# Performance work log

Hardware: AMD Instinct MI355X
Metric: run time of the kernel (lower is better)

The kernel has to match this reference:

```python
import jax, jax.numpy as jnp
import numpy as np
import math

EPS_LN = 1e-5
TARGET_ACTIVITY = 0.1
THETA = 2.0 ** 16

B, NH, T, D, N = 2, 12, 2048, 768, 256


def layernorm(x):
    m = jnp.mean(x, axis=-1, keepdims=True)
    v = jnp.mean((x - m) ** 2, axis=-1, keepdims=True)
    return (x - m) / jnp.sqrt(v + EPS_LN)


def get_freqs(n):
    q = jnp.floor(jnp.arange(n, dtype=jnp.float32) / 2.0) * 2.0  # quantize by 2
    return 1.0 / (THETA ** (q / n)) / (2.0 * math.pi)


def rope(phases, v):
    ph = (phases % 1.0) * (2.0 * math.pi)
    c, s = jnp.cos(ph), jnp.sin(ph)
    even = v[..., 0::2]
    odd = v[..., 1::2]
    v_rot = jnp.stack((-odd, even), axis=-1).reshape(v.shape)  # interleaved rotate
    return v * c + v_rot * s


def setup_inputs() -> dict:
    key = jax.random.key(0)
    ks = jax.random.split(key, 5)
    std = 0.02
    return {
        "x": jax.random.normal(ks[0], (B, 1, T, D), dtype=jnp.float32),
        "encoder": jax.random.normal(ks[1], (NH, D, N), dtype=jnp.float32) * std,
        "encoder_v": jax.random.normal(ks[2], (NH, D, N), dtype=jnp.float32) * std,
        "decoder": jax.random.normal(ks[3], (NH * N, D), dtype=jnp.float32) * std,
        "scale": jnp.ones((D,), dtype=jnp.float32),
        "running_activity": jnp.ones((D,), dtype=jnp.float32) * TARGET_ACTIVITY,
    }


def reference(x, encoder, encoder_v, decoder, scale, running_activity):
    Bv, _, Tv, Dv = x.shape
    nh, _, Nv = encoder.shape

    # encode + ReLU sparsify: [B,1,T,D] @ [nh,D,N] -> [B,nh,T,N]
    x_latent = jnp.einsum('bztd,hdn->bhtn', x, encoder)
    x_sparse = jax.nn.relu(x_latent)

    # RoPE on Q=K=x_sparse
    freqs = get_freqs(Nv)  # [N]
    r_phases = jnp.arange(Tv, dtype=jnp.float32)[:, None] * freqs[None, :]  # [T,N]
    QR = rope(r_phases, x_sparse)
    KR = rope(r_phases, x_sparse)

    # non-softmax causal attention, strictly lower-triangular (diag=-1)
    scores = jnp.einsum('bhtn,bhsn->bhts', QR, KR)
    mask = jnp.tril(jnp.ones((Tv, Tv), dtype=scores.dtype), k=-1)
    scores = scores * mask
    yKV = jnp.einsum('bhts,bsd->bhtd', scores, x[:, 0])  # V = x

    yKV = layernorm(yKV)
    y_sparse = jax.nn.relu(jnp.einsum('bhtd,hdn->bhtn', yKV, encoder_v))
    xy_sparse = x_sparse * y_sparse  # [B,nh,T,N]; dropout=0 (eval)

    # [B,nh,T,N] -> [B,1,T,nh*N] @ [nh*N,D]
    flat = jnp.transpose(xy_sparse, (0, 2, 1, 3)).reshape(Bv, 1, Tv, nh * Nv)
    yMLP = flat @ decoder

    y = layernorm(yMLP)
    regulation = TARGET_ACTIVITY / (running_activity + 1e-6)
    y = y * jnp.sqrt(regulation) * scale

    return layernorm(x + y), xy_sparse
```

## Files before the change

### kernel.cpp

```cpp
#include <hip/hip_runtime.h>
#include <math.h>

#define TT 2048
#define DD 768
#define NN 256
#define NHH 12
#define BB 2
#define CH 512

typedef unsigned short u16;
typedef __attribute__((ext_vector_type(8))) short bf16x8;
typedef __attribute__((ext_vector_type(8))) unsigned short u16x8;
typedef __attribute__((ext_vector_type(4))) float f32x4;

static inline int imin(int a, int b) { return a < b ? a : b; }

__device__ __forceinline__ u16 f2b(float f) {
  union { float f; unsigned u; } a; a.f = f;
  unsigned r = a.u + 0x7FFF + ((a.u >> 16) & 1);
  return (u16)(r >> 16);
}
__device__ __forceinline__ float b2f(u16 h) {
  union { unsigned u; float f; } a; a.u = ((unsigned)h) << 16;
  return a.f;
}

__device__ __forceinline__ void async16(const void* g, void* l) {
  __builtin_amdgcn_global_load_lds(
      (const __attribute__((address_space(1))) unsigned*)g,
      (__attribute__((address_space(3))) unsigned*)l, 16, 0, 0);
}

#define KSWZ(row) (((row) >> 1) & 3)

__device__ __forceinline__ void stage128x32(
    const u16* __restrict__ gbase, size_t ld, u16* lds, int tid) {
  const int w = tid >> 6, l = tid & 63;
#pragma unroll
  for (int q = 0; q < 2; ++q) {
    const int row = w * 32 + q * 16 + (l >> 2);
    const int kc = ((l & 3) ^ KSWZ(row)) << 3;
    async16(gbase + (size_t)row * ld + kc, lds + (w * 32 + q * 16) * 32);
  }
}

__device__ __forceinline__ void stage64x32(
    const u16* __restrict__ gbase, size_t ld, u16* lds, int tid) {
  const int w = tid >> 6, l = tid & 63;
  const int row = w * 16 + (l >> 2);
  const int kc = ((l & 3) ^ KSWZ(row)) << 3;
  async16(gbase + (size_t)row * ld + kc, lds + w * 512);
}

__device__ __forceinline__ void mfma_step(
    const u16* As, const u16* Bs, int wr, int wc, int lane, f32x4 acc[4][4]) {
  const int m16 = lane & 15, quad = lane >> 4;
  bf16x8 a[4], b[4];
#pragma unroll
  for (int i = 0; i < 4; ++i) {
    const int row = wr * 64 + i * 16 + m16;
    a[i] = *(const bf16x8*)&As[row * 32 + ((quad ^ KSWZ(row)) << 3)];
  }
#pragma unroll
  for (int j = 0; j < 4; ++j) {
    const int row = wc * 64 + j * 16 + m16;
    b[j] = *(const bf16x8*)&Bs[row * 32 + ((quad ^ KSWZ(row)) << 3)];
  }
#pragma unroll
  for (int i = 0; i < 4; ++i)
#pragma unroll
    for (int j = 0; j < 4; ++j)
      acc[i][j] = __builtin_amdgcn_mfma_f32_16x16x32_bf16(a[i], b[j], acc[i][j], 0, 0, 0);
}

__device__ __forceinline__ void copy_out128(
    const u16* buf, u16* g, size_t ld, int tid) {
#pragma unroll
  for (int s = 0; s < 8; ++s) {
    const int off = (s * 256 + tid) * 8;
    const int row = off >> 7, col = off & 127;
    *(u16x8*)&g[(size_t)row * ld + col] = *(const u16x8*)&buf[off];
  }
}

#define GEMM_PROLOGUE()                                            \
  __shared__ __attribute__((aligned(16))) u16 smem[32768];         \
  const int tid = threadIdx.x;                                     \
  const int w = tid >> 6, lane = tid & 63;                         \
  const int wr = w >> 1, wc = w & 1;                               \
  const int col16 = lane & 15, quad = lane >> 4;                   \
  f32x4 acc[4][4];                                                 \
  _Pragma("unroll") for (int i = 0; i < 4; ++i)                    \
  _Pragma("unroll") for (int j = 0; j < 4; ++j)                    \
      acc[i][j] = (f32x4){0.f, 0.f, 0.f, 0.f};

#define PIPELINED_K_LOOP64(ABASE, ALD, BBASE, BLD, KTOT)                    \
  {                                                                         \
    stage128x32((ABASE), (ALD), smem, tid);                                 \
    stage128x32((ABASE) + 32, (ALD), smem + 4096, tid);                     \
    stage128x32((BBASE), (BLD), smem + 8192, tid);                          \
    stage128x32((BBASE) + 32, (BLD), smem + 12288, tid);                    \
    const int np_ = (KTOT) / 64;                                            \
    for (int pp_ = 0; pp_ < np_; ++pp_) {                                   \
      u16* cb_ = (pp_ & 1) ? smem + 16384 : smem;                           \
      u16* nb_ = (pp_ & 1) ? smem : smem + 16384;                           \
      if (pp_ + 1 < np_) {                                                  \
        const int kn_ = (pp_ + 1) * 64;                                     \
        stage128x32((ABASE) + kn_, (ALD), nb_, tid);                        \
        stage128x32((ABASE) + kn_ + 32, (ALD), nb_ + 4096, tid);            \
        stage128x32((BBASE) + kn_, (BLD), nb_ + 8192, tid);                 \
        stage128x32((BBASE) + kn_ + 32, (BLD), nb_ + 12288, tid);           \
        asm volatile("s_waitcnt vmcnt(8)" ::: "memory");                    \
      } else {                                                              \
        asm volatile("s_waitcnt vmcnt(0)" ::: "memory");                    \
      }                                                                     \
      __builtin_amdgcn_s_barrier();                                         \
      __builtin_amdgcn_sched_barrier(0);                                    \
      mfma_step(cb_, cb_ + 8192, wr, wc, lane, acc);                        \
      mfma_step(cb_ + 4096, cb_ + 12288, wr, wc, lane, acc);                \
      __builtin_amdgcn_sched_barrier(0);                                    \
      __builtin_amdgcn_s_barrier();                                         \
    }                                                                       \
  }

__device__ __forceinline__ void tcvt_body(
    const float* __restrict__ ip, u16* __restrict__ op, int R, int C,
    int bx, int by, int tid, float (*tile)[33]) {
  const int c0 = bx * 32, r0 = by * 32;
  const int tx = tid & 31, ty = tid >> 5;
#pragma unroll
  for (int p = 0; p < 4; ++p)
    tile[ty + p * 8][tx] = ip[(size_t)(r0 + ty + p * 8) * C + c0 + tx];
  __syncthreads();
#pragma unroll
  for (int p = 0; p < 4; ++p)
    op[(size_t)(c0 + ty + p * 8) * R + r0 + tx] = f2b(tile[tx][ty + p * 8]);
}

__global__ __launch_bounds__(256) void k_prep(
    const float* __restrict__ x, u16* __restrict__ X16, u16* __restrict__ XT16,
    const float* __restrict__ enc, u16* __restrict__ ENCT,
    const float* __restrict__ encv, u16* __restrict__ ENCVT,
    const float* __restrict__ dec, u16* __restrict__ DECT,
    float2* __restrict__ CS) {
  __shared__ float tile[32][33];
  const int tid = threadIdx.x;
  const int bid = blockIdx.x;
  if (bid < 3072) {
    const size_t i = ((size_t)bid * 256 + tid) * 4;
    float4 v = *(const float4*)&x[i];
    u16 o[4] = {f2b(v.x), f2b(v.y), f2b(v.z), f2b(v.w)};
    *(ushort4*)&X16[i] = *(ushort4*)o;
  } else if (bid < 6144) {
    const int b = bid - 3072;
    const int bz = b / 1536, rb = b % 1536;
    tcvt_body(x + (size_t)bz * TT * DD, XT16 + (size_t)bz * DD * TT,
              TT, DD, rb % 24, rb / 24, tid, tile);
  } else if (bid < 8448) {
    const int b = bid - 6144;
    const int bz = b / 192, rb = b % 192;
    tcvt_body(enc + (size_t)bz * DD * NN, ENCT + (size_t)bz * NN * DD,
              DD, NN, rb % 8, rb / 8, tid, tile);
  } else if (bid < 10752) {
    const int b = bid - 8448;
    const int bz = b / 192, rb = b % 192;
    tcvt_body(encv + (size_t)bz * DD * NN, ENCVT + (size_t)bz * NN * DD,
              DD, NN, rb % 8, rb / 8, tid, tile);
  } else if (bid < 13056) {
    const int b = bid - 10752;
    tcvt_body(dec, DECT, NHH * NN, DD, b % 24, b / 24, tid, tile);
  } else {
    const int idx = (bid - 13056) * 256 + tid;
    const int t = idx >> 7, n2 = idx & 127;
    const float freq = exp2f((float)(2 * n2) * -0.0625f) * 0.15915494309189535f;
    const float phase = (float)t * freq;
    const float ph = (phase - floorf(phase)) * 6.283185307179586f;
    CS[idx] = make_float2(__cosf(ph), __sinf(ph));
  }
}

__global__ __launch_bounds__(256) void k_colsum(
    const u16* __restrict__ encvt, float* __restrict__ colsum) {
  const int row = blockIdx.x * 4 + (threadIdx.x >> 6);
  const int lane = threadIdx.x & 63;
  const u16* pr = encvt + (size_t)row * DD;
  float s = 0.f;
#pragma unroll
  for (int i = 0; i < 3; ++i) {
    ushort4 v = *(const ushort4*)&pr[(lane << 2) + i * 256];
    s += b2f(v.x) + b2f(v.y) + b2f(v.z) + b2f(v.w);
  }
#pragma unroll
  for (int off = 32; off; off >>= 1) s += __shfl_xor(s, off);
  if (lane == 0) colsum[row] = s;
}

__device__ __forceinline__ int swz8(int row) { return ((row >> 3) & 7) << 3; }

__global__ __launch_bounds__(256) void k1_encode(
    const u16* __restrict__ x16, const u16* __restrict__ enct,
    const float2* __restrict__ CS,
    u16* __restrict__ qr16, u16* __restrict__ qrt16) {
  const int h = blockIdx.z;
  const int m0 = blockIdx.x * 128, n0 = blockIdx.y * 128;
  GEMM_PROLOGUE();
  PIPELINED_K_LOOP64(x16 + (size_t)m0 * DD, DD,
                     enct + ((size_t)h * NN + n0) * DD, DD, DD);
  __syncthreads();
#pragma unroll
  for (int i = 0; i < 4; ++i)
#pragma unroll
    for (int j = 0; j < 4; ++j) {
      const int n = n0 + wc * 64 + j * 16 + col16;
      float rv[4], pv[4];
#pragma unroll
      for (int r = 0; r < 4; ++r) rv[r] = fmaxf(acc[i][j][r], 0.f);
#pragma unroll
      for (int r = 0; r < 4; ++r) pv[r] = __shfl_xor(rv[r], 1);
#pragma unroll
      for (int r = 0; r < 4; ++r) {
        const int lrow = wr * 64 + i * 16 + quad * 4 + r;
        const int t = (m0 + lrow) & (TT - 1);
        const float2 cs = CS[t * 128 + (n >> 1)];
        const float o = (n & 1) ? (rv[r] * cs.x + pv[r] * cs.y)
                                : (rv[r] * cs.x - pv[r] * cs.y);
        smem[lrow * 128 + ((wc * 64 + j * 16 + col16) ^ swz8(lrow))] = f2b(o);
      }
    }
  __syncthreads();
  const int bq = m0 >> 11, tb = m0 & (TT - 1);
  const size_t sl = (size_t)(bq * NHH + h);
  u16* qg = qr16 + (sl * TT + tb) * NN + n0;
#pragma unroll
  for (int s = 0; s < 8; ++s) {
    const int off = (s * 256 + tid) * 8;
    const int row = off >> 7, col = off & 127;
    *(u16x8*)&qg[(size_t)row * NN + col] =
        *(const u16x8*)&smem[row * 128 + (col ^ swz8(row))];
  }
#pragma unroll
  for (int s = 0; s < 8; ++s) {
    const int off = (s * 256 + tid) * 8;
    const int nr = off >> 7, tc = off & 127;
    const int sw = swz8(tc);
    u16 vals[8];
#pragma unroll
    for (int k = 0; k < 8; ++k) vals[k] = smem[(tc + k) * 128 + (nr ^ sw)];
    *(u16x8*)&qrt16[(sl * NN + n0 + nr) * TT + tb + tc] = *(u16x8*)vals;
  }
}

__global__ __launch_bounds__(256) void kS_band(
    const u16* __restrict__ qr16, u16* __restrict__ sb, int bh0) {
  const int z = blockIdx.y;
  const int bh = bh0 + z;
  const int cc = blockIdx.x / 10, rr = blockIdx.x % 10;
  int i = (int)((sqrtf(8.f * rr + 1.f) - 1.f) * 0.5f);
  while ((i + 1) * (i + 2) / 2 <= rr) ++i;
  while (i * (i + 1) / 2 > rr) --i;
  const int j = rr - i * (i + 1) / 2;
  const int t0 = (cc * 4 + i) * 128;
  const int s0 = cc * CH + j * 128;
  const u16* q = qr16 + (size_t)bh * TT * NN;
  GEMM_PROLOGUE();
  PIPELINED_K_LOOP64(q + (size_t)t0 * NN, NN, q + (size_t)s0 * NN, NN, NN);
  const bool diag = (i == j);
  __syncthreads();
#pragma unroll
  for (int ii = 0; ii < 4; ++ii)
#pragma unroll
    for (int jj = 0; jj < 4; ++jj) {
      const int s = s0 + wc * 64 + jj * 16 + col16;
#pragma unroll
      for (int r = 0; r < 4; ++r) {
        const int lrow = wr * 64 + ii * 16 + quad * 4 + r;
        const int t = t0 + lrow;
        float v = acc[ii][jj][r];
        if (diag && s >= t) v = 0.f;
        smem[lrow * 128 + wc * 64 + jj * 16 + col16] = f2b(v);
      }
    }
  __syncthreads();
  copy_out128(smem, sb + ((size_t)z * TT + t0) * CH + j * 128, CH, tid);
}

__global__ __launch_bounds__(256) void kB_all(
    const u16* __restrict__ xt16, const u16* __restrict__ qrt16,
    u16* __restrict__ h16, int bh0) {
  __shared__ __attribute__((aligned(16))) u16 sm[32768];
  u16* buf0 = sm;
  u16* buf1 = sm + 12288;
  u16* snap = sm + 24576;
  const int tid = threadIdx.x;
  const int w = tid >> 6, lane = tid & 63;
  const int m16 = lane & 15, quad = lane >> 4;
  const int z = blockIdx.z;
  const int bh = bh0 + z, b = bh / NHH;
  const int d0 = blockIdx.x * 64, n0 = blockIdx.y * 128;
  f32x4 acc[4][2];
#pragma unroll
  for (int i = 0; i < 4; ++i)
#pragma unroll
    for (int j = 0; j < 2; ++j) acc[i][j] = (f32x4){0.f, 0.f, 0.f, 0.f};
  const u16* Ab = xt16 + ((size_t)b * DD + d0) * TT;
  const u16* Bb = qrt16 + ((size_t)bh * NN + n0) * TT;
#define KB_STAGE(buf, k0)                                                   \
  {                                                                         \
    stage64x32(Ab + (k0), TT, (buf), tid);                                  \
    stage64x32(Ab + (k0) + 32, TT, (buf) + 2048, tid);                      \
    stage128x32(Bb + (k0), TT, (buf) + 4096, tid);                          \
    stage128x32(Bb + (k0) + 32, TT, (buf) + 8192, tid);                     \
  }
  for (int c = 0; c < 3; ++c) {
    const int kbase = c * CH;
    KB_STAGE(buf0, kbase);
    for (int s = 0; s < CH / 64; ++s) {
      u16* cb = (s & 1) ? buf1 : buf0;
      u16* nb = (s & 1) ? buf0 : buf1;
      if (s + 1 < CH / 64) {
        KB_STAGE(nb, kbase + (s + 1) * 64);
        asm volatile("s_waitcnt vmcnt(6)" ::: "memory");
      } else {
        asm volatile("s_waitcnt vmcnt(0)" ::: "memory");
      }
      __builtin_amdgcn_s_barrier();
      __builtin_amdgcn_sched_barrier(0);
#pragma unroll
      for (int half = 0; half < 2; ++half) {
        bf16x8 a[4], bb[2];
#pragma unroll
        for (int i = 0; i < 4; ++i) {
          const int row = i * 16 + m16;
          a[i] = *(const bf16x8*)&cb[half * 2048 + row * 32 +
                                     ((quad ^ KSWZ(row)) << 3)];
        }
#pragma unroll
        for (int j = 0; j < 2; ++j) {
          const int row = w * 32 + j * 16 + m16;
          bb[j] = *(const bf16x8*)&cb[4096 + half * 4096 + row * 32 +
                                      ((quad ^ KSWZ(row)) << 3)];
        }
#pragma unroll
        for (int i = 0; i < 4; ++i)
#pragma unroll
          for (int j = 0; j < 2; ++j)
            acc[i][j] = __builtin_amdgcn_mfma_f32_16x16x32_bf16(a[i], bb[j], acc[i][j], 0, 0, 0);
      }
      __builtin_amdgcn_sched_barrier(0);
      __builtin_amdgcn_s_barrier();
    }
#pragma unroll
    for (int i = 0; i < 4; ++i)
#pragma unroll
      for (int j = 0; j < 2; ++j)
#pragma unroll
        for (int r = 0; r < 4; ++r)
          snap[(i * 16 + quad * 4 + r) * 128 + w * 32 + j * 16 + m16] =
              f2b(acc[i][j][r]);
    __syncthreads();
    u16* hd = h16 + (size_t)(z * 3 + c) * DD * NN;
#pragma unroll
    for (int s4 = 0; s4 < 4; ++s4) {
      const int off = (s4 * 256 + tid) * 8;
      const int row = off >> 7, col = off & 127;
      *(u16x8*)&hd[(size_t)(d0 + row) * NN + n0 + col] = *(const u16x8*)&snap[off];
    }
    __syncthreads();
  }
#undef KB_STAGE
}

__device__ static const int TTORD[16] = {15, 11, 7, 14, 10, 6, 13, 9,
                                         5, 3, 12, 8, 4, 2, 1, 0};

__global__ __launch_bounds__(256) void kA_attn(
    const u16* __restrict__ qr16, const u16* __restrict__ h16,
    const u16* __restrict__ sb, const u16* __restrict__ xt16,
    u16* __restrict__ ykv16, float2* __restrict__ PART, int gsTT, int bh0) {
  __shared__ __attribute__((aligned(16))) u16 smem[32768];
  const int tid = threadIdx.x;
  const int w = tid >> 6, lane = tid & 63;
  const int wr = w >> 1, wc = w & 1;
  const int col16 = lane & 15, quad = lane >> 4;
  const int nwg = gridDim.x;
  const int bid = blockIdx.x;
  const int qn = nwg >> 3, r8 = nwg & 7;
  const int xcd = bid & 7, pos = bid >> 3;
  const int wg = (xcd < r8 ? xcd * (qn + 1) : r8 * (qn + 1) + (xcd - r8) * qn) + pos;
  const int z = wg / 96;
  const int tt = TTORD[(wg / 6) & 15];
  const int dblk = wg % 6;
  const int d0 = dblk * 128;
  const int bh = bh0 + z, b = bh / NHH;
  const int c = tt >> 2, it = tt & 3;
  const int t0 = tt * 128;
  f32x4 acc[4][4];
#pragma unroll
  for (int i = 0; i < 4; ++i)
#pragma unroll
    for (int j = 0; j < 4; ++j) acc[i][j] = (f32x4){0.f, 0.f, 0.f, 0.f};

  const int c4 = (c > 0) ? 4 : 0;
  const int nP = c4 + (it + 1) * 2;
  const u16* hs = h16 + ((size_t)(z * 3 + (c > 0 ? c - 1 : 0)) * DD + d0) * NN;
  const u16* qb = qr16 + ((size_t)bh * TT + t0) * NN;
  const u16* sbb = sb + ((size_t)z * TT + t0) * CH;
  const u16* xb = xt16 + ((size_t)b * DD + d0) * TT + c * CH;

#define KA_STAGE(buf, p)                                                  \
  {                                                                       \
    const u16 *pa_, *pb_; size_t la_, lb_;                                \
    if ((p) < c4) {                                                       \
      pa_ = qb + (p) * 64; la_ = NN;                                      \
      pb_ = hs + (p) * 64; lb_ = NN;                                      \
    } else {                                                              \
      const int q_ = (p) - c4;                                            \
      const int j_ = q_ >> 1, kk_ = (q_ & 1) << 6;                        \
      pa_ = sbb + j_ * 128 + kk_; la_ = CH;                               \
      pb_ = xb + j_ * 128 + kk_; lb_ = TT;                                \
    }                                                                     \
    stage128x32(pa_, la_, (buf), tid);                                    \
    stage128x32(pa_ + 32, la_, (buf) + 4096, tid);                        \
    stage128x32(pb_, lb_, (buf) + 8192, tid);                             \
    stage128x32(pb_ + 32, lb_, (buf) + 12288, tid);                       \
  }

  u16* bufA = smem;
  u16* bufB = smem + 16384;
  KA_STAGE(bufA, 0);
  for (int p = 0; p < nP; ++p) {
    u16* cb = (p & 1) ? bufB : bufA;
    u16* nb = (p & 1) ? bufA : bufB;
    if (p + 1 < nP) {
      KA_STAGE(nb, p + 1);
      asm volatile("s_waitcnt vmcnt(8)" ::: "memory");
    } else {
      asm volatile("s_waitcnt vmcnt(0)" ::: "memory");
    }
    __builtin_amdgcn_s_barrier();
    __builtin_amdgcn_sched_barrier(0);
    mfma_step(cb, cb + 8192, wr, wc, lane, acc);
    mfma_step(cb + 4096, cb + 12288, wr, wc, lane, acc);
    __builtin_amdgcn_sched_barrier(0);
    __builtin_amdgcn_s_barrier();
  }
#undef KA_STAGE

  __syncthreads();
#pragma unroll
  for (int i = 0; i < 4; ++i)
#pragma unroll
    for (int j = 0; j < 4; ++j)
#pragma unroll
      for (int r = 0; r < 4; ++r) {
        const int lrow = wr * 64 + i * 16 + quad * 4 + r;
        smem[lrow * 128 + wc * 64 + j * 16 + col16] = f2b(acc[i][j][r]);
      }
  __syncthreads();
  float2* scratch = (float2*)&smem[16384];
  u16* yg = ykv16 + ((size_t)z * TT + t0) * DD + d0;
#pragma unroll
  for (int s = 0; s < 8; ++s) {
    const int off = (s * 256 + tid) * 8;
    const int row = off >> 7, col = off & 127;
    const u16x8 v = *(const u16x8*)&smem[off];
    *(u16x8*)&yg[(size_t)row * DD + col] = v;
    float ps = 0.f, pq = 0.f;
#pragma unroll
    for (int k = 0; k < 8; ++k) {
      const float f = b2f(v[k]);
      ps += f;
      pq += f * f;
    }
    scratch[row * 17 + (tid & 15)] = make_float2(ps, pq);
  }
  __syncthreads();
  if (tid < 128) {
    const float2* pr = &scratch[tid * 17];
    float s = 0.f, q2 = 0.f;
#pragma unroll
    for (int k = 0; k < 16; ++k) { s += pr[k].x; q2 += pr[k].y; }
    PART[(size_t)dblk * gsTT + z * TT + t0 + tid] = make_float2(s, q2);
  }
}

__global__ __launch_bounds__(256) void k3r_stats(
    const float2* __restrict__ PART, float* __restrict__ mu,
    float* __restrict__ rs, int gsTT) {
  const int row = blockIdx.x * 256 + threadIdx.x;
  float s = 0.f, q = 0.f;
#pragma unroll
  for (int d = 0; d < 6; ++d) {
    const float2 p2 = PART[(size_t)d * gsTT + row];
    s += p2.x;
    q += p2.y;
  }
  const float m = s * (1.f / 768.f);
  mu[row] = m;
  rs[row] = rsqrtf(q * (1.f / 768.f) - m * m + 1e-5f);
}

__global__ __launch_bounds__(256) void k4_xy(
    const u16* __restrict__ ykv16, const u16* __restrict__ encvt,
    const float2* __restrict__ CS,
    u16* __restrict__ qrxy, const float* __restrict__ mu,
    const float* __restrict__ rs, const float* __restrict__ colsum,
    float* __restrict__ out2, int bh0) {
  const int z = blockIdx.z;
  const int bh = bh0 + z, h = bh % NHH;
  const int t0 = blockIdx.x * 128, n0 = blockIdx.y * 128;
  GEMM_PROLOGUE();
  PIPELINED_K_LOOP64(ykv16 + ((size_t)z * TT + t0) * DD, DD,
                     encvt + ((size_t)h * NN + n0) * DD, DD, DD);
  {
    const u16* qg = qrxy + ((size_t)bh * TT + t0) * NN + n0;
#pragma unroll
    for (int s = 0; s < 8; ++s) {
      const int row = s * 16 + w * 4 + (lane >> 4);
      const int col = (lane & 15) * 8;
      async16(qg + (size_t)row * NN + col,
              smem + 16384 + (s * 256 + w * 64) * 8);
    }
  }
  asm volatile("s_waitcnt vmcnt(0)" ::: "memory");
  __syncthreads();
#pragma unroll
  for (int i = 0; i < 4; ++i) {
    float muv[4], rsv[4];
#pragma unroll
    for (int r = 0; r < 4; ++r) {
      const int grow = z * TT + t0 + wr * 64 + i * 16 + quad * 4 + r;
      muv[r] = mu[grow];
      rsv[r] = rs[grow];
    }
#pragma unroll
    for (int j = 0; j < 4; ++j) {
      const int lcol = wc * 64 + j * 16 + col16;
      const int n = n0 + lcol;
      const float csum = colsum[h * NN + n];
#pragma unroll
      for (int r = 0; r < 4; ++r) {
        const int lrow = wr * 64 + i * 16 + quad * 4 + r;
        const int t = t0 + lrow;
        const float ys = fmaxf(rsv[r] * acc[i][j][r] - rsv[r] * muv[r] * csum, 0.f);
        const unsigned pq =
            *(const unsigned*)&smem[16384 + lrow * 128 + (lcol & ~1)];
        const float lo = b2f((u16)pq), hi = b2f((u16)(pq >> 16));
        const float2 cs = CS[t * 128 + (n >> 1)];
        const float xs = (n & 1) ? (hi * cs.x - lo * cs.y)
                                 : (lo * cs.x + hi * cs.y);
        const float val = ys * xs;
        out2[((size_t)bh * TT + t) * NN + n] = val;
        smem[lrow * 128 + lcol] = f2b(val);
      }
    }
  }
  __syncthreads();
  copy_out128(smem, qrxy + ((size_t)bh * TT + t0) * NN + n0, NN, tid);
}

__global__ __launch_bounds__(256) void k5_mlp(
    const u16* __restrict__ xyq, const u16* __restrict__ dect,
    float* __restrict__ ymlp) {
  __shared__ __attribute__((aligned(16))) u16 sm[24576];
  const int tid = threadIdx.x;
  const int w = tid >> 6, lane = tid & 63;
  const int wr = w >> 1, wc = w & 1;
  const int m16 = lane & 15, quad = lane >> 4;
  const int m0 = blockIdx.x * 64, d0 = blockIdx.y * 64;
  f32x4 acc[2][2];
#pragma unroll
  for (int i = 0; i < 2; ++i)
#pragma unroll
    for (int j = 0; j < 2; ++j) acc[i][j] = (f32x4){0.f, 0.f, 0.f, 0.f};
  const int ar = w * 16 + (lane >> 2);
  const int m = m0 + ar;
  const int b = m >> 11, t = m & (TT - 1);
  const int kc = (((lane & 3) ^ KSWZ(ar)) << 3);
#define K5_STAGE(buf, k0)                                                   \
  {                                                                         \
    const int hh_ = (k0) >> 8;                                              \
    const int kk_ = ((k0) & 255) + kc;                                      \
    const u16* ap_ = xyq + ((size_t)(b * NHH + hh_) * TT + t) * NN;         \
    async16(ap_ + kk_, (buf) + w * 512);                                    \
    async16(ap_ + kk_ + 32, (buf) + 2048 + w * 512);                        \
    stage64x32(dect + (size_t)d0 * (NHH * NN) + (k0), NHH * NN,             \
               (buf) + 4096, tid);                                          \
    stage64x32(dect + (size_t)d0 * (NHH * NN) + (k0) + 32, NHH * NN,        \
               (buf) + 6144, tid);                                          \
  }
  const int NK = (NHH * NN) / 64;
  u16 *b0 = sm, *b1 = sm + 8192, *b2 = sm + 16384;
  K5_STAGE(b0, 0);
  K5_STAGE(b1, 64);
  for (int s = 0; s < NK; ++s) {
    if (s + 2 < NK) {
      K5_STAGE(b2, (s + 2) * 64);
      asm volatile("s_waitcnt vmcnt(8)" ::: "memory");
    } else if (s + 1 < NK) {
      asm volatile("s_waitcnt vmcnt(4)" ::: "memory");
    } else {
      asm volatile("s_waitcnt vmcnt(0)" ::: "memory");
    }
    __builtin_amdgcn_s_barrier();
    __builtin_amdgcn_sched_barrier(0);
#pragma unroll
    for (int half = 0; half < 2; ++half) {
      bf16x8 a[2], bb[2];
#pragma unroll
      for (int i = 0; i < 2; ++i) {
        const int row = wr * 32 + i * 16 + m16;
        a[i] = *(const bf16x8*)&b0[half * 2048 + row * 32 +
                                   ((quad ^ KSWZ(row)) << 3)];
      }
#pragma unroll
      for (int j = 0; j < 2; ++j) {
        const int row = wc * 32 + j * 16 + m16;
        bb[j] = *(const bf16x8*)&b0[4096 + half * 2048 + row * 32 +
                                    ((quad ^ KSWZ(row)) << 3)];
      }
#pragma unroll
      for (int i = 0; i < 2; ++i)
#pragma unroll
        for (int j = 0; j < 2; ++j)
          acc[i][j] = __builtin_amdgcn_mfma_f32_16x16x32_bf16(a[i], bb[j], acc[i][j], 0, 0, 0);
    }
    __builtin_amdgcn_sched_barrier(0);
    __builtin_amdgcn_s_barrier();
    u16* tmp = b0; b0 = b1; b1 = b2; b2 = tmp;
  }
#undef K5_STAGE
#pragma unroll
  for (int i = 0; i < 2; ++i)
#pragma unroll
    for (int j = 0; j < 2; ++j) {
      const int d = d0 + wc * 32 + j * 16 + m16;
#pragma unroll
      for (int r = 0; r < 4; ++r) {
        const int mm = m0 + wr * 32 + i * 16 + quad * 4 + r;
        ymlp[(size_t)mm * DD + d] = acc[i][j][r];
      }
    }
}

__global__ __launch_bounds__(256) void k6_final(
    const float* __restrict__ ymlp, const float* __restrict__ x,
    const float* __restrict__ scale, const float* __restrict__ ra,
    float* __restrict__ out1) {
  const int row = blockIdx.x;
  const int tid = threadIdx.x;
  const int wid = tid >> 6, lane = tid & 63;
  __shared__ float red[8];
  float v[3];
  float sum = 0.f, sq = 0.f;
#pragma unroll
  for (int j = 0; j < 3; ++j) {
    v[j] = ymlp[(size_t)row * DD + tid + j * 256];
    sum += v[j]; sq += v[j] * v[j];
  }
#pragma unroll
  for (int off = 32; off; off >>= 1) { sum += __shfl_xor(sum, off); sq += __shfl_xor(sq, off); }
  if (lane == 0) { red[wid] = sum; red[4 + wid] = sq; }
  __syncthreads();
  sum = red[0] + red[1] + red[2] + red[3];
  sq = red[4] + red[5] + red[6] + red[7];
  const float m1 = sum * (1.f / 768.f);
  const float r1 = rsqrtf(sq * (1.f / 768.f) - m1 * m1 + 1e-5f);
  float z[3];
  float sum2 = 0.f, sq2 = 0.f;
#pragma unroll
  for (int j = 0; j < 3; ++j) {
    const int d = tid + j * 256;
    float y = (v[j] - m1) * r1 * sqrtf(0.1f / (ra[d] + 1e-6f)) * scale[d];
    z[j] = x[(size_t)row * DD + d] + y;
    sum2 += z[j]; sq2 += z[j] * z[j];
  }
  __syncthreads();
#pragma unroll
  for (int off = 32; off; off >>= 1) { sum2 += __shfl_xor(sum2, off); sq2 += __shfl_xor(sq2, off); }
  if (lane == 0) { red[wid] = sum2; red[4 + wid] = sq2; }
  __syncthreads();
  sum2 = red[0] + red[1] + red[2] + red[3];
  sq2 = red[4] + red[5] + red[6] + red[7];
  const float m2 = sum2 * (1.f / 768.f);
  const float r2 = rsqrtf(sq2 * (1.f / 768.f) - m2 * m2 + 1e-5f);
#pragma unroll
  for (int j = 0; j < 3; ++j)
    out1[(size_t)row * DD + tid + j * 256] = (z[j] - m2) * r2;
}

extern "C" void kernel_launch(void* const* d_in, const int* in_sizes, int n_in,
                              void* d_out, int out_size, void* d_ws, size_t ws_size,
                              hipStream_t stream) {
  const float* x = (const float*)d_in[0];
  const float* enc = (const float*)d_in[1];
  const float* encv = (const float*)d_in[2];
  const float* dec = (const float*)d_in[3];
  const float* scale = (const float*)d_in[4];
  const float* ra = (const float*)d_in[5];
  float* out1 = (float*)d_out;
  float* out2 = out1 + (size_t)BB * TT * DD;
  float* ymlp = out1;

  const int NS = BB * NHH;
  unsigned char* p = (unsigned char*)d_ws;
  u16* X16 = (u16*)p;    p += (size_t)BB * TT * DD * 2;
  u16* XT16 = (u16*)p;   p += (size_t)BB * DD * TT * 2;
  u16* ENCT = (u16*)p;   p += (size_t)NHH * NN * DD * 2;
  u16* ENCVT = (u16*)p;  p += (size_t)NHH * NN * DD * 2;
  u16* DECT = (u16*)p;   p += (size_t)DD * NHH * NN * 2;
  u16* QR16 = (u16*)p;   p += (size_t)NS * TT * NN * 2;
  u16* QRT16 = (u16*)p;  p += (size_t)NS * NN * TT * 2;
  float* COLSUM = (float*)p; p += (size_t)NHH * NN * 4;
  float2* CS = (float2*)p;   p += (size_t)TT * (NN / 2) * sizeof(float2);
  const size_t SLICE_B = (size_t)TT * CH * 2 + 3 * (size_t)DD * NN * 2 +
                         (size_t)TT * DD * 2 + (size_t)TT * 56;
  size_t fixed = (size_t)(p - (unsigned char*)d_ws);
  size_t rem = (ws_size > fixed) ? ws_size - fixed : 0;
  int GSmax = (int)(rem / SLICE_B);
  if (GSmax < 1) GSmax = 1;
  if (GSmax > NS) GSmax = NS;
  const int ngrp = (NS + GSmax - 1) / GSmax;
  const int GS = (NS + ngrp - 1) / ngrp;
  u16* SB = (u16*)p;     p += (size_t)GS * TT * CH * 2;
  u16* H16 = (u16*)p;    p += (size_t)GS * 3 * DD * NN * 2;
  u16* YKV16 = (u16*)p;  p += (size_t)GS * TT * DD * 2;
  float2* PART = (float2*)p; p += (size_t)GS * TT * 6 * sizeof(float2);
  float* MU = (float*)p; p += (size_t)GS * TT * 4;
  float* RS = (float*)p; p += (size_t)GS * TT * 4;
  const int gsTT = GS * TT;

  k_prep<<<dim3(14080), 256, 0, stream>>>(
      x, X16, XT16, enc, ENCT, encv, ENCVT, dec, DECT, CS);
  k_colsum<<<dim3(NHH * NN / 4), 256, 0, stream>>>(ENCVT, COLSUM);

  k1_encode<<<dim3(BB * TT / 128, NN / 128, NHH), 256, 0, stream>>>(
      X16, ENCT, CS, QR16, QRT16);

  for (int bh0 = 0; bh0 < NS; bh0 += GS) {
    const int gs = imin(GS, NS - bh0);
    kS_band<<<dim3(40, gs), 256, 0, stream>>>(QR16, SB, bh0);
    kB_all<<<dim3(DD / 64, NN / 128, gs), 256, 0, stream>>>(
        XT16, QRT16, H16, bh0);
    kA_attn<<<dim3(96 * gs), 256, 0, stream>>>(
        QR16, H16, SB, XT16, YKV16, PART, gsTT, bh0);
    k3r_stats<<<dim3(gs * TT / 256), 256, 0, stream>>>(PART, MU, RS, gsTT);
    k4_xy<<<dim3(TT / 128, NN / 128, gs), 256, 0, stream>>>(
        YKV16, ENCVT, CS, QR16, MU, RS, COLSUM, out2, bh0);
  }

  k5_mlp<<<dim3(BB * TT / 64, DD / 64), 256, 0, stream>>>(QR16, DECT, ymlp);
  k6_final<<<dim3(BB * TT), 256, 0, stream>>>(ymlp, x, scale, ra, out1);
}
```

Measured before the change: 356.2 us.

## Merge band and H kernels, fold stats into k4, retile MLP GEMM

Combines the banded score kernel and the H-projection kernel into a single launch that dispatches on block index, so their blocks share the GPU and one launch is saved. It removes the separate row-statistics kernel by having k4_xy reduce the six partial sums itself, which drops the MU/RS buffers. It also retiles the decoder MLP GEMM from 64x64 to 128x128 tiles with double buffering and a swizzled block order. The trade-offs are redundant partial-sum reads in k4, fewer MLP blocks (192), and a mixed-workload kernel whose blocks run different code paths.

```diff
diff --git a/kernel.cpp b/kernel.cpp
--- a/kernel.cpp
+++ b/kernel.cpp
@@ -83,8 +83,10 @@
   }
 }
 
-#define GEMM_PROLOGUE()                                            \
-  __shared__ __attribute__((aligned(16))) u16 smem[32768];         \
+#define GEMM_SMEM \
+  __shared__ __attribute__((aligned(16))) u16 smem[32768];
+
+#define GEMM_VARS()                                                \
   const int tid = threadIdx.x;                                     \
   const int w = tid >> 6, lane = tid & 63;                         \
   const int wr = w >> 1, wc = w & 1;                               \
@@ -93,6 +95,8 @@
   _Pragma("unroll") for (int i = 0; i < 4; ++i)                    \
   _Pragma("unroll") for (int j = 0; j < 4; ++j)                    \
       acc[i][j] = (f32x4){0.f, 0.f, 0.f, 0.f};
+
+#define GEMM_PROLOGUE() GEMM_SMEM GEMM_VARS()
 
 #define PIPELINED_K_LOOP64(ABASE, ALD, BBASE, BLD, KTOT)                    \
   {                                                                         \
@@ -250,60 +254,65 @@
   }
 }
 
-__global__ __launch_bounds__(256) void kS_band(
-    const u16* __restrict__ qr16, u16* __restrict__ sb, int bh0) {
-  const int z = blockIdx.y;
-  const int bh = bh0 + z;
-  const int cc = blockIdx.x / 10, rr = blockIdx.x % 10;
-  int i = (int)((sqrtf(8.f * rr + 1.f) - 1.f) * 0.5f);
-  while ((i + 1) * (i + 2) / 2 <= rr) ++i;
-  while (i * (i + 1) / 2 > rr) --i;
-  const int j = rr - i * (i + 1) / 2;
-  const int t0 = (cc * 4 + i) * 128;
-  const int s0 = cc * CH + j * 128;
-  const u16* q = qr16 + (size_t)bh * TT * NN;
-  GEMM_PROLOGUE();
-  PIPELINED_K_LOOP64(q + (size_t)t0 * NN, NN, q + (size_t)s0 * NN, NN, NN);
-  const bool diag = (i == j);
-  __syncthreads();
-#pragma unroll
-  for (int ii = 0; ii < 4; ++ii)
-#pragma unroll
-    for (int jj = 0; jj < 4; ++jj) {
-      const int s = s0 + wc * 64 + jj * 16 + col16;
-#pragma unroll
-      for (int r = 0; r < 4; ++r) {
-        const int lrow = wr * 64 + ii * 16 + quad * 4 + r;
-        const int t = t0 + lrow;
-        float v = acc[ii][jj][r];
-        if (diag && s >= t) v = 0.f;
-        smem[lrow * 128 + wc * 64 + jj * 16 + col16] = f2b(v);
-      }
-    }
-  __syncthreads();
-  copy_out128(smem, sb + ((size_t)z * TT + t0) * CH + j * 128, CH, tid);
-}
-
-__global__ __launch_bounds__(256) void kB_all(
-    const u16* __restrict__ xt16, const u16* __restrict__ qrt16,
-    u16* __restrict__ h16, int bh0) {
-  __shared__ __attribute__((aligned(16))) u16 sm[32768];
-  u16* buf0 = sm;
-  u16* buf1 = sm + 12288;
-  u16* snap = sm + 24576;
+__global__ __launch_bounds__(256) void kSB(
+    const u16* __restrict__ qr16, const u16* __restrict__ xt16,
+    const u16* __restrict__ qrt16, u16* __restrict__ sb,
+    u16* __restrict__ h16, int nS, int bh0) {
+  GEMM_SMEM;
   const int tid = threadIdx.x;
   const int w = tid >> 6, lane = tid & 63;
-  const int m16 = lane & 15, quad = lane >> 4;
-  const int z = blockIdx.z;
-  const int bh = bh0 + z, b = bh / NHH;
-  const int d0 = blockIdx.x * 64, n0 = blockIdx.y * 128;
-  f32x4 acc[4][2];
-#pragma unroll
-  for (int i = 0; i < 4; ++i)
-#pragma unroll
-    for (int j = 0; j < 2; ++j) acc[i][j] = (f32x4){0.f, 0.f, 0.f, 0.f};
-  const u16* Ab = xt16 + ((size_t)b * DD + d0) * TT;
-  const u16* Bb = qrt16 + ((size_t)bh * NN + n0) * TT;
+  const int col16 = lane & 15, quad = lane >> 4;
+  if ((int)blockIdx.x < nS) {
+    const int wr = w >> 1, wc = w & 1;
+    const int z = blockIdx.x / 40, sub = blockIdx.x % 40;
+    const int bh = bh0 + z;
+    const int cc = sub / 10, rr = sub % 10;
+    int i = (int)((sqrtf(8.f * rr + 1.f) - 1.f) * 0.5f);
+    while ((i + 1) * (i + 2) / 2 <= rr) ++i;
+    while (i * (i + 1) / 2 > rr) --i;
+    const int j = rr - i * (i + 1) / 2;
+    const int t0 = (cc * 4 + i) * 128;
+    const int s0 = cc * CH + j * 128;
+    const u16* q = qr16 + (size_t)bh * TT * NN;
+    f32x4 acc[4][4];
+#pragma unroll
+    for (int a = 0; a < 4; ++a)
+#pragma unroll
+      for (int b = 0; b < 4; ++b) acc[a][b] = (f32x4){0.f, 0.f, 0.f, 0.f};
+    PIPELINED_K_LOOP64(q + (size_t)t0 * NN, NN, q + (size_t)s0 * NN, NN, NN);
+    const bool diag = (i == j);
+    __syncthreads();
+#pragma unroll
+    for (int ii = 0; ii < 4; ++ii)
+#pragma unroll
+      for (int jj = 0; jj < 4; ++jj) {
+        const int s = s0 + wc * 64 + jj * 16 + col16;
+#pragma unroll
+        for (int r = 0; r < 4; ++r) {
+          const int lrow = wr * 64 + ii * 16 + quad * 4 + r;
+          const int t = t0 + lrow;
+          float v = acc[ii][jj][r];
+          if (diag && s >= t) v = 0.f;
+          smem[lrow * 128 + wc * 64 + jj * 16 + col16] = f2b(v);
+        }
+      }
+    __syncthreads();
+    copy_out128(smem, sb + ((size_t)z * TT + t0) * CH + j * 128, CH, tid);
+  } else {
+    const int r2 = blockIdx.x - nS;
+    const int z = r2 / 24, rr2 = r2 % 24;
+    const int d0 = (rr2 % 12) * 64, n0 = (rr2 / 12) * 128;
+    const int bh = bh0 + z, b = bh / NHH;
+    u16* buf0 = smem;
+    u16* buf1 = smem + 12288;
+    u16* snap = smem + 24576;
+    f32x4 acc[4][2];
+#pragma unroll
+    for (int i = 0; i < 4; ++i)
+#pragma unroll
+      for (int j = 0; j < 2; ++j) acc[i][j] = (f32x4){0.f, 0.f, 0.f, 0.f};
+    const u16* Ab = xt16 + ((size_t)b * DD + d0) * TT;
+    const u16* Bb = qrt16 + ((size_t)bh * NN + n0) * TT;
 #define KB_STAGE(buf, k0)                                                   \
   {                                                                         \
     stage64x32(Ab + (k0), TT, (buf), tid);                                  \
@@ -311,63 +320,64 @@
     stage128x32(Bb + (k0), TT, (buf) + 4096, tid);                          \
     stage128x32(Bb + (k0) + 32, TT, (buf) + 8192, tid);                     \
   }
-  for (int c = 0; c < 3; ++c) {
-    const int kbase = c * CH;
-    KB_STAGE(buf0, kbase);
-    for (int s = 0; s < CH / 64; ++s) {
-      u16* cb = (s & 1) ? buf1 : buf0;
-      u16* nb = (s & 1) ? buf0 : buf1;
-      if (s + 1 < CH / 64) {
-        KB_STAGE(nb, kbase + (s + 1) * 64);
-        asm volatile("s_waitcnt vmcnt(6)" ::: "memory");
-      } else {
-        asm volatile("s_waitcnt vmcnt(0)" ::: "memory");
+    for (int c = 0; c < 3; ++c) {
+      const int kbase = c * CH;
+      KB_STAGE(buf0, kbase);
+      for (int s = 0; s < CH / 64; ++s) {
+        u16* cb = (s & 1) ? buf1 : buf0;
+        u16* nb = (s & 1) ? buf0 : buf1;
+        if (s + 1 < CH / 64) {
+          KB_STAGE(nb, kbase + (s + 1) * 64);
+          asm volatile("s_waitcnt vmcnt(6)" ::: "memory");
+        } else {
+          asm volatile("s_waitcnt vmcnt(0)" ::: "memory");
+        }
+        __builtin_amdgcn_s_barrier();
+        __builtin_amdgcn_sched_barrier(0);
+#pragma unroll
+        for (int half = 0; half < 2; ++half) {
+          bf16x8 a[4], bb[2];
+#pragma unroll
+          for (int i = 0; i < 4; ++i) {
+            const int row = i * 16 + col16;
+            a[i] = *(const bf16x8*)&cb[half * 2048 + row * 32 +
+                                       ((quad ^ KSWZ(row)) << 3)];
+          }
+#pragma unroll
+          for (int j = 0; j < 2; ++j) {
+            const int row = w * 32 + j * 16 + col16;
+            bb[j] = *(const bf16x8*)&cb[4096 + half * 4096 + row * 32 +
+                                        ((quad ^ KSWZ(row)) << 3)];
+          }
+#pragma unroll
+          for (int i = 0; i < 4; ++i)
+#pragma unroll
+            for (int j = 0; j < 2; ++j)
+              acc[i][j] = __builtin_amdgcn_mfma_f32_16x16x32_bf16(a[i], bb[j], acc[i][j], 0, 0, 0);
+        }
+        __builtin_amdgcn_sched_barrier(0);
+        __builtin_amdgcn_s_barrier();
       }
-      __builtin_amdgcn_s_barrier();
-      __builtin_amdgcn_sched_barrier(0);
-#pragma unroll
-      for (int half = 0; half < 2; ++half) {
-        bf16x8 a[4], bb[2];
-#pragma unroll
-        for (int i = 0; i < 4; ++i) {
-          const int row = i * 16 + m16;
-          a[i] = *(const bf16x8*)&cb[half * 2048 + row * 32 +
-                                     ((quad ^ KSWZ(row)) << 3)];
-        }
-#pragma unroll
-        for (int j = 0; j < 2; ++j) {
-          const int row = w * 32 + j * 16 + m16;
-          bb[j] = *(const bf16x8*)&cb[4096 + half * 4096 + row * 32 +
-                                      ((quad ^ KSWZ(row)) << 3)];
-        }
-#pragma unroll
-        for (int i = 0; i < 4; ++i)
-#pragma unroll
-          for (int j = 0; j < 2; ++j)
-            acc[i][j] = __builtin_amdgcn_mfma_f32_16x16x32_bf16(a[i], bb[j], acc[i][j], 0, 0, 0);
+#pragma unroll
+      for (int i = 0; i < 4; ++i)
+#pragma unroll
+        for (int j = 0; j < 2; ++j)
+#pragma unroll
+          for (int r = 0; r < 4; ++r)
+            snap[(i * 16 + quad * 4 + r) * 128 + w * 32 + j * 16 + col16] =
+                f2b(acc[i][j][r]);
+      __syncthreads();
+      u16* hd = h16 + (size_t)(z * 3 + c) * DD * NN;
+#pragma unroll
+      for (int s4 = 0; s4 < 4; ++s4) {
+        const int off = (s4 * 256 + tid) * 8;
+        const int row = off >> 7, col = off & 127;
+        *(u16x8*)&hd[(size_t)(d0 + row) * NN + n0 + col] = *(const u16x8*)&snap[off];
       }
-      __builtin_amdgcn_sched_barrier(0);
-      __builtin_amdgcn_s_barrier();
-    }
-#pragma unroll
-    for (int i = 0; i < 4; ++i)
-#pragma unroll
-      for (int j = 0; j < 2; ++j)
-#pragma unroll
-        for (int r = 0; r < 4; ++r)
-          snap[(i * 16 + quad * 4 + r) * 128 + w * 32 + j * 16 + m16] =
-              f2b(acc[i][j][r]);
-    __syncthreads();
-    u16* hd = h16 + (size_t)(z * 3 + c) * DD * NN;
-#pragma unroll
-    for (int s4 = 0; s4 < 4; ++s4) {
-      const int off = (s4 * 256 + tid) * 8;
-      const int row = off >> 7, col = off & 127;
-      *(u16x8*)&hd[(size_t)(d0 + row) * NN + n0 + col] = *(const u16x8*)&snap[off];
-    }
-    __syncthreads();
-  }
+      __syncthreads();
+    }
 #undef KB_STAGE
+  }
 }
 
 __device__ static const int TTORD[16] = {15, 11, 7, 14, 10, 6, 13, 9,
@@ -377,7 +387,7 @@
     const u16* __restrict__ qr16, const u16* __restrict__ h16,
     const u16* __restrict__ sb, const u16* __restrict__ xt16,
     u16* __restrict__ ykv16, float2* __restrict__ PART, int gsTT, int bh0) {
-  __shared__ __attribute__((aligned(16))) u16 smem[32768];
+  GEMM_SMEM;
   const int tid = threadIdx.x;
   const int w = tid >> 6, lane = tid & 63;
   const int wr = w >> 1, wc = w & 1;
@@ -484,28 +494,12 @@
   }
 }
 
-__global__ __launch_bounds__(256) void k3r_stats(
-    const float2* __restrict__ PART, float* __restrict__ mu,
-    float* __restrict__ rs, int gsTT) {
-  const int row = blockIdx.x * 256 + threadIdx.x;
-  float s = 0.f, q = 0.f;
-#pragma unroll
-  for (int d = 0; d < 6; ++d) {
-    const float2 p2 = PART[(size_t)d * gsTT + row];
-    s += p2.x;
-    q += p2.y;
-  }
-  const float m = s * (1.f / 768.f);
-  mu[row] = m;
-  rs[row] = rsqrtf(q * (1.f / 768.f) - m * m + 1e-5f);
-}
-
 __global__ __launch_bounds__(256) void k4_xy(
     const u16* __restrict__ ykv16, const u16* __restrict__ encvt,
     const float2* __restrict__ CS,
-    u16* __restrict__ qrxy, const float* __restrict__ mu,
-    const float* __restrict__ rs, const float* __restrict__ colsum,
-    float* __restrict__ out2, int bh0) {
+    u16* __restrict__ qrxy, const float2* __restrict__ PART,
+    const float* __restrict__ colsum,
+    float* __restrict__ out2, int gsTT, int bh0) {
   const int z = blockIdx.z;
   const int bh = bh0 + z, h = bh % NHH;
   const int t0 = blockIdx.x * 128, n0 = blockIdx.y * 128;
@@ -530,8 +524,16 @@
 #pragma unroll
     for (int r = 0; r < 4; ++r) {
       const int grow = z * TT + t0 + wr * 64 + i * 16 + quad * 4 + r;
-      muv[r] = mu[grow];
-      rsv[r] = rs[grow];
+      float s_ = 0.f, q_ = 0.f;
+#pragma unroll
+      for (int d = 0; d < 6; ++d) {
+        const float2 p2 = PART[(size_t)d * gsTT + grow];
+        s_ += p2.x;
+        q_ += p2.y;
+      }
+      const float m_ = s_ * (1.f / 768.f);
+      muv[r] = m_;
+      rsv[r] = rsqrtf(q_ * (1.f / 768.f) - m_ * m_ + 1e-5f);
     }
 #pragma unroll
     for (int j = 0; j < 4; ++j) {
@@ -562,82 +564,50 @@
 __global__ __launch_bounds__(256) void k5_mlp(
     const u16* __restrict__ xyq, const u16* __restrict__ dect,
     float* __restrict__ ymlp) {
-  __shared__ __attribute__((aligned(16))) u16 sm[24576];
-  const int tid = threadIdx.x;
-  const int w = tid >> 6, lane = tid & 63;
-  const int wr = w >> 1, wc = w & 1;
-  const int m16 = lane & 15, quad = lane >> 4;
-  const int m0 = blockIdx.x * 64, d0 = blockIdx.y * 64;
-  f32x4 acc[2][2];
-#pragma unroll
-  for (int i = 0; i < 2; ++i)
-#pragma unroll
-    for (int j = 0; j < 2; ++j) acc[i][j] = (f32x4){0.f, 0.f, 0.f, 0.f};
-  const int ar = w * 16 + (lane >> 2);
-  const int m = m0 + ar;
-  const int b = m >> 11, t = m & (TT - 1);
-  const int kc = (((lane & 3) ^ KSWZ(ar)) << 3);
-#define K5_STAGE(buf, k0)                                                   \
+  GEMM_PROLOGUE();
+  const int bid = blockIdx.x;
+  const int wg = (bid & 7) * 24 + (bid >> 3);
+  const int m0 = (wg / 6) * 128, d0 = (wg % 6) * 128;
+  const int b = m0 >> 11, t0 = m0 & (TT - 1);
+#define K5_ST(buf, p)                                                       \
   {                                                                         \
-    const int hh_ = (k0) >> 8;                                              \
-    const int kk_ = ((k0) & 255) + kc;                                      \
-    const u16* ap_ = xyq + ((size_t)(b * NHH + hh_) * TT + t) * NN;         \
-    async16(ap_ + kk_, (buf) + w * 512);                                    \
-    async16(ap_ + kk_ + 32, (buf) + 2048 + w * 512);                        \
-    stage64x32(dect + (size_t)d0 * (NHH * NN) + (k0), NHH * NN,             \
-               (buf) + 4096, tid);                                          \
-    stage64x32(dect + (size_t)d0 * (NHH * NN) + (k0) + 32, NHH * NN,        \
-               (buf) + 6144, tid);                                          \
-  }
-  const int NK = (NHH * NN) / 64;
-  u16 *b0 = sm, *b1 = sm + 8192, *b2 = sm + 16384;
-  K5_STAGE(b0, 0);
-  K5_STAGE(b1, 64);
-  for (int s = 0; s < NK; ++s) {
-    if (s + 2 < NK) {
-      K5_STAGE(b2, (s + 2) * 64);
+    const int k0_ = (p) * 64, hh_ = k0_ >> 8, kk_ = k0_ & 255;              \
+    const u16* pa_ = xyq + ((size_t)(b * NHH + hh_) * TT + t0) * NN + kk_;  \
+    const u16* pb_ = dect + (size_t)d0 * (NHH * NN) + k0_;                  \
+    stage128x32(pa_, NN, (buf), tid);                                       \
+    stage128x32(pa_ + 32, NN, (buf) + 4096, tid);                           \
+    stage128x32(pb_, NHH * NN, (buf) + 8192, tid);                          \
+    stage128x32(pb_ + 32, NHH * NN, (buf) + 12288, tid);                    \
+  }
+  const int NP = (NHH * NN) / 64;
+  u16* bufA = smem;
+  u16* bufB = smem + 16384;
+  K5_ST(bufA, 0);
+  for (int p = 0; p < NP; ++p) {
+    u16* cb = (p & 1) ? bufB : bufA;
+    u16* nb = (p & 1) ? bufA : bufB;
+    if (p + 1 < NP) {
+      K5_ST(nb, p + 1);
       asm volatile("s_waitcnt vmcnt(8)" ::: "memory");
-    } else if (s + 1 < NK) {
-      asm volatile("s_waitcnt vmcnt(4)" ::: "memory");
     } else {
       asm volatile("s_waitcnt vmcnt(0)" ::: "memory");
     }
     __builtin_amdgcn_s_barrier();
     __builtin_amdgcn_sched_barrier(0);
-#pragma unroll
-    for (int half = 0; half < 2; ++half) {
-      bf16x8 a[2], bb[2];
-#pragma unroll
-      for (int i = 0; i < 2; ++i) {
-        const int row = wr * 32 + i * 16 + m16;
-        a[i] = *(const bf16x8*)&b0[half * 2048 + row * 32 +
-                                   ((quad ^ KSWZ(row)) << 3)];
-      }
-#pragma unroll
-      for (int j = 0; j < 2; ++j) {
-        const int row = wc * 32 + j * 16 + m16;
-        bb[j] = *(const bf16x8*)&b0[4096 + half * 2048 + row * 32 +
-                                    ((quad ^ KSWZ(row)) << 3)];
-      }
-#pragma unroll
-      for (int i = 0; i < 2; ++i)
-#pragma unroll
-        for (int j = 0; j < 2; ++j)
-          acc[i][j] = __builtin_amdgcn_mfma_f32_16x16x32_bf16(a[i], bb[j], acc[i][j], 0, 0, 0);
-    }
+    mfma_step(cb, cb + 8192, wr, wc, lane, acc);
+    mfma_step(cb + 4096, cb + 12288, wr, wc, lane, acc);
     __builtin_amdgcn_sched_barrier(0);
     __builtin_amdgcn_s_barrier();
-    u16* tmp = b0; b0 = b1; b1 = b2; b2 = tmp;
-  }
-#undef K5_STAGE
-#pragma unroll
-  for (int i = 0; i < 2; ++i)
-#pragma unroll
-    for (int j = 0; j < 2; ++j) {
-      const int d = d0 + wc * 32 + j * 16 + m16;
+  }
+#undef K5_ST
+#pragma unroll
+  for (int i = 0; i < 4; ++i)
+#pragma unroll
+    for (int j = 0; j < 4; ++j) {
+      const int d = d0 + wc * 64 + j * 16 + col16;
 #pragma unroll
       for (int r = 0; r < 4; ++r) {
-        const int mm = m0 + wr * 32 + i * 16 + quad * 4 + r;
+        const int mm = m0 + wr * 64 + i * 16 + quad * 4 + r;
         ymlp[(size_t)mm * DD + d] = acc[i][j][r];
       }
     }
@@ -714,7 +684,7 @@
   float* COLSUM = (float*)p; p += (size_t)NHH * NN * 4;
   float2* CS = (float2*)p;   p += (size_t)TT * (NN / 2) * sizeof(float2);
   const size_t SLICE_B = (size_t)TT * CH * 2 + 3 * (size_t)DD * NN * 2 +
-                         (size_t)TT * DD * 2 + (size_t)TT * 56;
+                         (size_t)TT * DD * 2 + (size_t)TT * 48;
   size_t fixed = (size_t)(p - (unsigned char*)d_ws);
   size_t rem = (ws_size > fixed) ? ws_size - fixed : 0;
   int GSmax = (int)(rem / SLICE_B);
@@ -726,8 +696,6 @@
   u16* H16 = (u16*)p;    p += (size_t)GS * 3 * DD * NN * 2;
   u16* YKV16 = (u16*)p;  p += (size_t)GS * TT * DD * 2;
   float2* PART = (float2*)p; p += (size_t)GS * TT * 6 * sizeof(float2);
-  float* MU = (float*)p; p += (size_t)GS * TT * 4;
-  float* RS = (float*)p; p += (size_t)GS * TT * 4;
   const int gsTT = GS * TT;
 
   k_prep<<<dim3(14080), 256, 0, stream>>>(
@@ -739,16 +707,14 @@
 
   for (int bh0 = 0; bh0 < NS; bh0 += GS) {
     const int gs = imin(GS, NS - bh0);
-    kS_band<<<dim3(40, gs), 256, 0, stream>>>(QR16, SB, bh0);
-    kB_all<<<dim3(DD / 64, NN / 128, gs), 256, 0, stream>>>(
-        XT16, QRT16, H16, bh0);
+    kSB<<<dim3(64 * gs), 256, 0, stream>>>(
+        QR16, XT16, QRT16, SB, H16, 40 * gs, bh0);
     kA_attn<<<dim3(96 * gs), 256, 0, stream>>>(
         QR16, H16, SB, XT16, YKV16, PART, gsTT, bh0);
-    k3r_stats<<<dim3(gs * TT / 256), 256, 0, stream>>>(PART, MU, RS, gsTT);
     k4_xy<<<dim3(TT / 128, NN / 128, gs), 256, 0, stream>>>(
-        YKV16, ENCVT, CS, QR16, MU, RS, COLSUM, out2, bh0);
-  }
-
-  k5_mlp<<<dim3(BB * TT / 64, DD / 64), 256, 0, stream>>>(QR16, DECT, ymlp);
+        YKV16, ENCVT, CS, QR16, PART, COLSUM, out2, gsTT, bh0);
+  }
+
+  k5_mlp<<<dim3(192), 256, 0, stream>>>(QR16, DECT, ymlp);
   k6_final<<<dim3(BB * TT), 256, 0, stream>>>(ymlp, x, scale, ra, out1);
 }
```

After: 353.0 us. About the same (-0.9%).
